# Optimization experiments

Hardware: AMD Instinct MI355X
Metric: run time of the kernel (lower is better)

Reference implementation:

```python
import jax, jax.numpy as jnp
import numpy as np

B, N, E, D = 8, 8192, 1024, 256

def setup_inputs() -> dict:
    key = jax.random.key(0)
    ks = jax.random.split(key, 6)
    obs = jax.random.normal(ks[0], (B, N, D), dtype=jnp.float32)
    mask_flat = (jax.random.uniform(ks[1], (B, N)) > 0.1).astype(jnp.float32)
    idx = jax.random.randint(ks[2], (B, N), 0, E)
    # incidence[b, e, n] = 1 iff obs n belongs to variable e (consistent with idx)
    incidence = jnp.transpose(jax.nn.one_hot(idx, E, dtype=jnp.float32), (0, 2, 1))
    # params (random instead of the degenerate zero-init so the math is exercised)
    w_m = jax.random.normal(ks[3], (1, 2 * D), dtype=jnp.float32) * 0.02
    b_m = jnp.full((1,), 3.0, dtype=jnp.float32)
    w_e = jax.random.normal(ks[4], (D // 4, 2 * D), dtype=jnp.float32) * 0.02
    b_e = jnp.zeros((D // 4,), dtype=jnp.float32)
    return {"obs": obs, "mask_flat": mask_flat,
            "variable_incidence_matrix": incidence,
            "variable_indices_flattened": idx,
            "w_m": w_m, "b_m": b_m, "w_e": w_e, "b_e": b_e}

def reference(obs, mask_flat, variable_incidence_matrix, variable_indices_flattened,
              w_m, b_m, w_e, b_e):
    # mean of member-obs embeddings per variable (hyperedge): (B,E,D)
    var_count = jnp.clip(variable_incidence_matrix.sum(-1, keepdims=True), 1.0, None)
    var_context = jnp.einsum('ben,bnd->bed', variable_incidence_matrix, obs) / var_count
    # gather each obs node's variable context: (B,N,D)
    obs_var_ctx = jax.vmap(lambda v, i: v[i])(var_context, variable_indices_flattened)
    membrane_input = jnp.concatenate([obs, obs - obs_var_ctx], axis=-1)  # (B,N,2D)
    membrane = (membrane_input @ w_m.T + b_m)[..., 0]                    # (B,N)
    g_n = jax.nn.sigmoid(membrane) * mask_flat
    e_n = (membrane_input @ w_e.T + b_e) * g_n[..., None] * mask_flat[..., None]
    return (g_n, e_n)
```

## Files before the change

### kernel.cpp

```cpp
#include <hip/hip_runtime.h>

#define B_ 8
#define N_ 8192
#define E_ 1024
#define ROWS (B_ * N_)
#define BE (B_ * E_)
#define NT 10
#define KT 8

typedef float  f32x4  __attribute__((ext_vector_type(4)));
typedef __bf16 bf16x8 __attribute__((ext_vector_type(8)));

#define SE16_OFF  0
#define SM16_OFF  (SE16_OFF + ROWS * 64 * 2)
#define Y2E_OFF   (SM16_OFF + ROWS * 2)
#define Y2M_OFF   (Y2E_OFF + ROWS * 64 * 2)
#define SEG_OFF   (Y2M_OFF + ROWS * 2)
#define ORD_OFF   (SEG_OFF + BE * 8)
#define WEF_OFF   (ORD_OFF + ROWS * 4)

__device__ inline float bflo(unsigned u) { return __uint_as_float(u << 16); }
__device__ inline float bfhi(unsigned u) { return __uint_as_float(u & 0xffff0000u); }

__global__ __launch_bounds__(1024) void bucketize_kernel(
    const int* __restrict__ idx, const float* __restrict__ we,
    const float* __restrict__ wm, char* __restrict__ ws) {

    const int bid = blockIdx.x;
    if (bid >= 8) {
        const int t = (bid - 8) * 1024 + threadIdx.x;
        if (t >= KT * NT * 64) return;
        __bf16* wef = (__bf16*)(ws + WEF_OFF);
        const int lane = t & 63;
        const int nt = (t >> 6) % NT;
        const int kt = t / (NT * 64);
        const int grp = nt / 5;
        const int r   = (nt % 5) * 16 + (lane & 15);
        const int k0  = kt * 32 + (lane >> 4) * 8;
        bf16x8 v;
#pragma unroll
        for (int i = 0; i < 8; ++i) {
            const int k = k0 + i;
            float f = 0.f;
            if (r < 64)       f = grp ? we[r * 512 + 256 + k] : we[r * 512 + k] + we[r * 512 + 256 + k];
            else if (r == 64) f = grp ? wm[256 + k]           : wm[k] + wm[256 + k];
            v[i] = (__bf16)f;
        }
        *(bf16x8*)(wef + (size_t)t * 8) = v;
        return;
    }

    __shared__ unsigned h[1024];
    __shared__ unsigned wpart[16];
    const int b = bid;
    const int t = threadIdx.x;
    const int lane = t & 63;
    const int w = t >> 6;

    h[t] = 0u;
    __syncthreads();

    unsigned my[8];
#pragma unroll
    for (int i = 0; i < 8; ++i) my[i] = (unsigned)idx[(b << 13) + (i << 10) + t];
#pragma unroll
    for (int i = 0; i < 8; ++i) atomicAdd(&h[my[i]], 1u);
    __syncthreads();

    const unsigned v = h[t];
    unsigned inc = v;
#pragma unroll
    for (int off = 1; off < 64; off <<= 1) {
        const unsigned u = __shfl_up(inc, off);
        if (lane >= off) inc += u;
    }
    if (lane == 63) wpart[w] = inc;
    __syncthreads();
    unsigned add = 0;
    for (int ww = 0; ww < w; ++ww) add += wpart[ww];
    const unsigned base = add + inc - v;

    ((uint2*)(ws + SEG_OFF))[(b << 10) + t] = (uint2){(unsigned)(b << 13) + base, v};
    __syncthreads();
    h[t] = base;
    __syncthreads();

    unsigned* order = (unsigned*)(ws + ORD_OFF);
#pragma unroll
    for (int i = 0; i < 8; ++i) {
        const unsigned p = atomicAdd(&h[my[i]], 1u);
        order[(b << 13) + p] = (unsigned)((b << 13) + (i << 10) + t);
    }
}

__global__ __launch_bounds__(256) void gemm_kernel(
    const float* __restrict__ obs, char* __restrict__ ws) {

    const __bf16*   wefg = (const __bf16*)(ws + WEF_OFF);
    const unsigned* ordu = (const unsigned*)(ws + ORD_OFF);
    const int tid = threadIdx.x;
    const int l   = tid & 63;
    const int pw0 = blockIdx.x * 128 + (tid >> 6) * 32;
    const int q8  = (l >> 4) << 3;

    const unsigned r0 = ordu[pw0 + (l & 15)];
    const unsigned r1 = ordu[pw0 + 16 + (l & 15)];

    f32x4 acc[2][NT];
#pragma unroll
    for (int a = 0; a < 2; ++a)
#pragma unroll
        for (int b = 0; b < NT; ++b) acc[a][b] = (f32x4){0.f, 0.f, 0.f, 0.f};

    const float* o0 = obs + (((size_t)r0) << 8) + q8;
    const float* o1 = obs + (((size_t)r1) << 8) + q8;

#pragma unroll
    for (int g = 0; g < KT; ++g) {
        const f32x4 oa0 = *(const f32x4*)(o0 + g * 32);
        const f32x4 ob0 = *(const f32x4*)(o0 + g * 32 + 4);
        const f32x4 oa1 = *(const f32x4*)(o1 + g * 32);
        const f32x4 ob1 = *(const f32x4*)(o1 + g * 32 + 4);
        bf16x8 A0, A1;
#pragma unroll
        for (int i = 0; i < 4; ++i) {
            A0[i] = (__bf16)oa0[i];  A0[4 + i] = (__bf16)ob0[i];
            A1[i] = (__bf16)oa1[i];  A1[4 + i] = (__bf16)ob1[i];
        }
#pragma unroll
        for (int nt = 0; nt < NT; ++nt) {
            const bf16x8 bb = *(const bf16x8*)(wefg + (size_t)(((g * NT + nt) << 6) + l) * 8);
            acc[0][nt] = __builtin_amdgcn_mfma_f32_16x16x32_bf16(A0, bb, acc[0][nt], 0, 0, 0);
            acc[1][nt] = __builtin_amdgcn_mfma_f32_16x16x32_bf16(A1, bb, acc[1][nt], 0, 0, 0);
        }
    }

    __bf16* sE  = (__bf16*)(ws + SE16_OFF);
    __bf16* sM  = (__bf16*)(ws + SM16_OFF);
    __bf16* y2e = (__bf16*)(ws + Y2E_OFF);
    __bf16* y2m = (__bf16*)(ws + Y2M_OFF);

    const int cgrp = (l >> 4) << 2;
    const int c16  = l & 15;
#pragma unroll
    for (int rt = 0; rt < 2; ++rt) {
#pragma unroll
        for (int j = 0; j < 4; ++j) {
            const int dp = pw0 + rt * 16 + cgrp + j;
#pragma unroll
            for (int nt = 0; nt < 4; ++nt) {
                sE [((size_t)dp << 6) + (nt << 4) + c16] = (__bf16)acc[rt][nt][j];
                y2e[((size_t)dp << 6) + (nt << 4) + c16] = (__bf16)acc[rt][5 + nt][j];
            }
            if (c16 == 0) {
                sM [dp] = (__bf16)acc[rt][4][j];
                y2m[dp] = (__bf16)acc[rt][9][j];
            }
        }
    }
}

__global__ __launch_bounds__(256) void tail_kernel(
    const float* __restrict__ mask, const float* __restrict__ bmp,
    const float* __restrict__ bep, const char* __restrict__ ws,
    float* __restrict__ out) {

    const int bucket = blockIdx.x * 4 + (threadIdx.x >> 6);
    const int l  = threadIdx.x & 63;
    const int lc = l & 31;
    const int hi = l >> 5;

    const uint2 sg = ((const uint2*)(ws + SEG_OFF))[bucket];
    const unsigned start = sg.x, len = sg.y;
    if (len == 0) return;

    const unsigned*       y2eu = (const unsigned*)(ws + Y2E_OFF);
    const unsigned short* y2m  = (const unsigned short*)(ws + Y2M_OFF);

    float ax = 0.f, ay = 0.f;
    for (unsigned i = hi; i < len; i += 2) {
        const unsigned u = y2eu[(size_t)(start + i) * 32 + lc];
        ax += bflo(u); ay += bfhi(u);
    }
    ax += __shfl_xor(ax, 32);
    ay += __shfl_xor(ay, 32);

    float mm = 0.f;
    for (unsigned i = l; i < len; i += 64) mm += bflo(y2m[start + i]);
#pragma unroll
    for (int off = 1; off < 64; off <<= 1) mm += __shfl_xor(mm, off);

    const float inv = 1.f / (float)len;
    const float meL = ax * inv, meH = ay * inv, mM = mm * inv;
    const float bm  = bmp[0];
    const float beL = bep[2 * lc], beH = bep[2 * lc + 1];

    const unsigned*       sEu  = (const unsigned*)(ws + SE16_OFF);
    const unsigned short* sM16 = (const unsigned short*)(ws + SM16_OFF);
    const unsigned*       ordu = (const unsigned*)(ws + ORD_OFF);

    for (unsigned i = hi; i < len; i += 2) {
        const unsigned d   = start + i;
        const unsigned row = ordu[d];
        const unsigned u   = sEu[(size_t)d * 32 + lc];
        const float sm = bflo(sM16[d]);
        const float mk = mask[row];
        const float m  = sm - mM + bm;
        const float g  = mk / (1.f + __expf(-m));
        float2 e;
        e.x = (bflo(u) - meL + beL) * g * mk;
        e.y = (bfhi(u) - meH + beH) * g * mk;
        *(float2*)(out + (size_t)ROWS + ((size_t)row << 6) + 2 * lc) = e;
        if (lc == 0) out[row] = g;
    }
}

extern "C" void kernel_launch(void* const* d_in, const int* in_sizes, int n_in,
                              void* d_out, int out_size, void* d_ws, size_t ws_size,
                              hipStream_t stream) {
    (void)in_sizes; (void)n_in; (void)out_size; (void)ws_size;
    const float* obs  = (const float*)d_in[0];
    const float* mask = (const float*)d_in[1];
    const int*   idx  = (const int*)d_in[3];
    const float* w_m  = (const float*)d_in[4];
    const float* b_m  = (const float*)d_in[5];
    const float* w_e  = (const float*)d_in[6];
    const float* b_e  = (const float*)d_in[7];

    char* ws = (char*)d_ws;

    bucketize_kernel<<<13, 1024, 0, stream>>>(idx, w_e, w_m, ws);
    gemm_kernel<<<ROWS / 128, 256, 0, stream>>>(obs, ws);
    tail_kernel<<<BE / 4, 256, 0, stream>>>(mask, b_m, b_e, ws, (float*)d_out);
}
```

Before: 45.95 us.

## Fuse segmented mean and epilogue into GEMM kernel with cross-block bucket reduction

Merges the tail kernel into the GEMM kernel. Per-bucket sums of the y2 projections are reduced in shared memory within each 128-row block, and the outputs are written directly for buckets fully contained in the block. Buckets that span block boundaries publish partial sums to a global slot array, and the last-arriving block (tracked with an atomic counter) finishes them serially. This removes the y2e/y2m workspace round-trip and one kernel launch. In exchange it adds a large LDS footprint, a serial loop for boundary buckets, and the correctness risk of relying on the last-block pattern.

```diff
diff --git a/kernel.cpp b/kernel.cpp
--- a/kernel.cpp
+++ b/kernel.cpp
@@ -13,18 +13,23 @@
 
 #define SE16_OFF  0
 #define SM16_OFF  (SE16_OFF + ROWS * 64 * 2)
-#define Y2E_OFF   (SM16_OFF + ROWS * 2)
-#define Y2M_OFF   (Y2E_OFF + ROWS * 64 * 2)
-#define SEG_OFF   (Y2M_OFF + ROWS * 2)
+#define SEG_OFF   (SM16_OFF + ROWS * 2)
 #define ORD_OFF   (SEG_OFF + BE * 8)
 #define WEF_OFF   (ORD_OFF + ROWS * 4)
-
-__device__ inline float bflo(unsigned u) { return __uint_as_float(u << 16); }
-__device__ inline float bfhi(unsigned u) { return __uint_as_float(u & 0xffff0000u); }
+#define GYS_OFF   (WEF_OFF + KT * NT * 64 * 8 * 2)
+#define GCNT_OFF  (GYS_OFF + (size_t)BE * 4 * 66 * 4)
+
+__device__ inline float bfu16(unsigned short u) { return __uint_as_float(((unsigned)u) << 16); }
 
 __global__ __launch_bounds__(1024) void bucketize_kernel(
     const int* __restrict__ idx, const float* __restrict__ we,
     const float* __restrict__ wm, char* __restrict__ ws) {
+
+    {
+        unsigned* gcnt = (unsigned*)(ws + GCNT_OFF);
+        const int gz = blockIdx.x * 1024 + threadIdx.x;
+        if (gz < BE) gcnt[gz] = 0u;
+    }
 
     const int bid = blockIdx.x;
     if (bid >= 8) {
@@ -93,18 +98,49 @@
     }
 }
 
-__global__ __launch_bounds__(256) void gemm_kernel(
-    const float* __restrict__ obs, char* __restrict__ ws) {
+__global__ __launch_bounds__(256) void gemm_fused_kernel(
+    const float* __restrict__ obs, const float* __restrict__ mask,
+    const int* __restrict__ idx, const float* __restrict__ bmp,
+    const float* __restrict__ bep, char* __restrict__ ws,
+    float* __restrict__ out) {
+
+    __shared__ float bsum[129][66];
 
     const __bf16*   wefg = (const __bf16*)(ws + WEF_OFF);
     const unsigned* ordu = (const unsigned*)(ws + ORD_OFF);
-    const int tid = threadIdx.x;
-    const int l   = tid & 63;
-    const int pw0 = blockIdx.x * 128 + (tid >> 6) * 32;
-    const int q8  = (l >> 4) << 3;
-
-    const unsigned r0 = ordu[pw0 + (l & 15)];
-    const unsigned r1 = ordu[pw0 + 16 + (l & 15)];
+    const uint2*    seg  = (const uint2*)(ws + SEG_OFF);
+    __bf16*   sE   = (__bf16*)(ws + SE16_OFF);
+    __bf16*   sM   = (__bf16*)(ws + SM16_OFF);
+    float*    gys  = (float*)(ws + GYS_OFF);
+    unsigned* gcnt = (unsigned*)(ws + GCNT_OFF);
+
+    const int tid    = threadIdx.x;
+    const int l      = tid & 63;
+    const int wv     = tid >> 6;
+    const int bstart = blockIdx.x * 128;
+    const int pw     = bstart + wv * 32;
+    const int c16    = l & 15;
+    const int cgrp   = (l >> 4) << 2;
+
+    for (int i = tid; i < 129 * 66; i += 256) (&bsum[0][0])[i] = 0.f;
+    __syncthreads();
+
+    unsigned row32 = 0; int bkt32 = -1; float mk32 = 0.f;
+    if (l < 32) {
+        row32 = ordu[pw + l];
+        bkt32 = (int)(((row32 >> 13) << 10) + (unsigned)idx[row32]);
+        mk32  = mask[row32];
+    }
+    const unsigned rA0 = __shfl(row32, c16);
+    const unsigned rA1 = __shfl(row32, 16 + c16);
+
+    const unsigned rowb0 = ordu[bstart];
+    const int kb0blk = (int)(((rowb0 >> 13) << 10) + (unsigned)idx[rowb0]);
+
+    const float bm = bmp[0];
+    float bel[4];
+#pragma unroll
+    for (int k = 0; k < 4; ++k) bel[k] = bep[(k << 4) + c16];
 
     f32x4 acc[2][NT];
 #pragma unroll
@@ -112,8 +148,9 @@
 #pragma unroll
         for (int b = 0; b < NT; ++b) acc[a][b] = (f32x4){0.f, 0.f, 0.f, 0.f};
 
-    const float* o0 = obs + (((size_t)r0) << 8) + q8;
-    const float* o1 = obs + (((size_t)r1) << 8) + q8;
+    const int q8 = (l >> 4) << 3;
+    const float* o0 = obs + (((size_t)rA0) << 8) + q8;
+    const float* o1 = obs + (((size_t)rA1) << 8) + q8;
 
 #pragma unroll
     for (int g = 0; g < KT; ++g) {
@@ -135,83 +172,124 @@
         }
     }
 
-    __bf16* sE  = (__bf16*)(ws + SE16_OFF);
-    __bf16* sM  = (__bf16*)(ws + SM16_OFF);
-    __bf16* y2e = (__bf16*)(ws + Y2E_OFF);
-    __bf16* y2m = (__bf16*)(ws + Y2M_OFF);
-
-    const int cgrp = (l >> 4) << 2;
-    const int c16  = l & 15;
-#pragma unroll
-    for (int rt = 0; rt < 2; ++rt) {
+    unsigned bmsk = 0;
+    float invrow[2][4] = {{0.f,0.f,0.f,0.f},{0.f,0.f,0.f,0.f}};
+    int s = 0;
+    while (s < 32) {
+        const int bkt = __shfl(bkt32, s);
+        const unsigned long long mrun = __ballot(bkt32 == bkt);
+        const unsigned long long mm = ~(mrun >> s);
+        const int e = s + (__ffsll((long long)mm) - 1);
+        const uint2 sg = seg[bkt];
+        const bool bnd = (sg.x < (unsigned)bstart) || (sg.x + sg.y > (unsigned)(bstart + 128));
+        const float invf = 1.f / (float)sg.y;
+        const int krel = bkt - kb0blk;
+
+        float s0 = 0.f, s1 = 0.f, s2 = 0.f, s3 = 0.f, sm5 = 0.f;
+#pragma unroll
+        for (int rt = 0; rt < 2; ++rt)
+#pragma unroll
+            for (int j = 0; j < 4; ++j) {
+                const int rr = rt * 16 + cgrp + j;
+                if (rr >= s && rr < e) {
+                    s0 += acc[rt][5][j]; s1 += acc[rt][6][j];
+                    s2 += acc[rt][7][j]; s3 += acc[rt][8][j];
+                    sm5 += acc[rt][9][j];
+                    invrow[rt][j] = invf;
+                    if (bnd) {
+                        bmsk |= 1u << (rt * 4 + j);
+                        const int pos = pw + rr;
+                        sE[((size_t)pos << 6) +  0 + c16] = (__bf16)acc[rt][0][j];
+                        sE[((size_t)pos << 6) + 16 + c16] = (__bf16)acc[rt][1][j];
+                        sE[((size_t)pos << 6) + 32 + c16] = (__bf16)acc[rt][2][j];
+                        sE[((size_t)pos << 6) + 48 + c16] = (__bf16)acc[rt][3][j];
+                        if (c16 == 0) sM[pos] = (__bf16)acc[rt][4][j];
+                    }
+                }
+            }
+        s0 += __shfl_xor(s0, 16); s0 += __shfl_xor(s0, 32);
+        s1 += __shfl_xor(s1, 16); s1 += __shfl_xor(s1, 32);
+        s2 += __shfl_xor(s2, 16); s2 += __shfl_xor(s2, 32);
+        s3 += __shfl_xor(s3, 16); s3 += __shfl_xor(s3, 32);
+        sm5 += __shfl_xor(sm5, 16); sm5 += __shfl_xor(sm5, 32);
+        if (l < 16) {
+            atomicAdd(&bsum[krel][ 0 + c16], s0);
+            atomicAdd(&bsum[krel][16 + c16], s1);
+            atomicAdd(&bsum[krel][32 + c16], s2);
+            atomicAdd(&bsum[krel][48 + c16], s3);
+            if (l == 0) atomicAdd(&bsum[krel][64], sm5);
+        }
+        s = e;
+    }
+    __syncthreads();
+
+#pragma unroll
+    for (int rt = 0; rt < 2; ++rt)
 #pragma unroll
         for (int j = 0; j < 4; ++j) {
-            const int dp = pw0 + rt * 16 + cgrp + j;
-#pragma unroll
-            for (int nt = 0; nt < 4; ++nt) {
-                sE [((size_t)dp << 6) + (nt << 4) + c16] = (__bf16)acc[rt][nt][j];
-                y2e[((size_t)dp << 6) + (nt << 4) + c16] = (__bf16)acc[rt][5 + nt][j];
+            const int rr = rt * 16 + cgrp + j;
+            const int krel = __shfl(bkt32, rr) - kb0blk;
+            const float invf = invrow[rt][j];
+            const float mM  = bsum[krel][64] * invf;
+            const float sMv = __shfl(acc[rt][4][j], l & 48);
+            const float mk  = __shfl(mk32, rr);
+            const unsigned row = __shfl(row32, rr);
+            const float g = mk / (1.f + __expf(-(sMv - mM + bm)));
+            if (!((bmsk >> (rt * 4 + j)) & 1u)) {
+                if (c16 == 0) out[row] = g;
+#pragma unroll
+                for (int k = 0; k < 4; ++k) {
+                    const float mean = bsum[krel][(k << 4) + c16] * invf;
+                    out[(size_t)ROWS + ((size_t)row << 6) + (k << 4) + c16] =
+                        (acc[rt][k][j] - mean + bel[k]) * g * mk;
+                }
             }
-            if (c16 == 0) {
-                sM [dp] = (__bf16)acc[rt][4][j];
-                y2m[dp] = (__bf16)acc[rt][9][j];
+        }
+
+    int kb = -1;
+    if (wv == 0) kb = kb0blk;
+    if (wv == 3) {
+        const int kbt = __shfl(bkt32, 31);
+        kb = (kbt == kb0blk) ? -1 : kbt;
+    }
+    if (kb >= 0) {
+        const uint2 sg = seg[kb];
+        if (sg.x < (unsigned)bstart || sg.x + sg.y > (unsigned)(bstart + 128)) {
+            const int krel   = kb - kb0blk;
+            const int firstb = (int)(sg.x >> 7);
+            const int nctr   = (int)((sg.x + sg.y - 1) >> 7) - firstb + 1;
+            const int slot   = (int)blockIdx.x - firstb;
+            float* slotp = gys + ((size_t)kb * 4 + slot) * 66;
+            slotp[l] = bsum[krel][l];
+            if (l == 0) slotp[64] = bsum[krel][64];
+            __threadfence();
+            unsigned old = 0;
+            if (l == 0) old = atomicAdd(&gcnt[kb], 1u);
+            old = __shfl(old, 0);
+            if ((int)old == nctr - 1) {
+                __threadfence();
+                float tot = 0.f, totM = 0.f;
+                for (int s2 = 0; s2 < nctr; ++s2) {
+                    const float* sp2 = gys + ((size_t)kb * 4 + s2) * 66;
+                    tot += sp2[l];
+                    if (l == 0) totM += sp2[64];
+                }
+                const float invf  = 1.f / (float)sg.y;
+                const float meanL = tot * invf;
+                const float meanM = __shfl(totM, 0) * invf;
+                const unsigned short* sEu = (const unsigned short*)sE;
+                const unsigned short* sMu = (const unsigned short*)sM;
+                for (unsigned p = sg.x; p < sg.x + sg.y; ++p) {
+                    const unsigned row = ordu[p];
+                    const float mk = mask[row];
+                    const float m  = bfu16(sMu[p]) - meanM + bm;
+                    const float g  = mk / (1.f + __expf(-m));
+                    out[(size_t)ROWS + ((size_t)row << 6) + l] =
+                        (bfu16(sEu[(size_t)p * 64 + l]) - meanL + bep[l]) * g * mk;
+                    if (l == 0) out[row] = g;
+                }
             }
         }
-    }
-}
-
-__global__ __launch_bounds__(256) void tail_kernel(
-    const float* __restrict__ mask, const float* __restrict__ bmp,
-    const float* __restrict__ bep, const char* __restrict__ ws,
-    float* __restrict__ out) {
-
-    const int bucket = blockIdx.x * 4 + (threadIdx.x >> 6);
-    const int l  = threadIdx.x & 63;
-    const int lc = l & 31;
-    const int hi = l >> 5;
-
-    const uint2 sg = ((const uint2*)(ws + SEG_OFF))[bucket];
-    const unsigned start = sg.x, len = sg.y;
-    if (len == 0) return;
-
-    const unsigned*       y2eu = (const unsigned*)(ws + Y2E_OFF);
-    const unsigned short* y2m  = (const unsigned short*)(ws + Y2M_OFF);
-
-    float ax = 0.f, ay = 0.f;
-    for (unsigned i = hi; i < len; i += 2) {
-        const unsigned u = y2eu[(size_t)(start + i) * 32 + lc];
-        ax += bflo(u); ay += bfhi(u);
-    }
-    ax += __shfl_xor(ax, 32);
-    ay += __shfl_xor(ay, 32);
-
-    float mm = 0.f;
-    for (unsigned i = l; i < len; i += 64) mm += bflo(y2m[start + i]);
-#pragma unroll
-    for (int off = 1; off < 64; off <<= 1) mm += __shfl_xor(mm, off);
-
-    const float inv = 1.f / (float)len;
-    const float meL = ax * inv, meH = ay * inv, mM = mm * inv;
-    const float bm  = bmp[0];
-    const float beL = bep[2 * lc], beH = bep[2 * lc + 1];
-
-    const unsigned*       sEu  = (const unsigned*)(ws + SE16_OFF);
-    const unsigned short* sM16 = (const unsigned short*)(ws + SM16_OFF);
-    const unsigned*       ordu = (const unsigned*)(ws + ORD_OFF);
-
-    for (unsigned i = hi; i < len; i += 2) {
-        const unsigned d   = start + i;
-        const unsigned row = ordu[d];
-        const unsigned u   = sEu[(size_t)d * 32 + lc];
-        const float sm = bflo(sM16[d]);
-        const float mk = mask[row];
-        const float m  = sm - mM + bm;
-        const float g  = mk / (1.f + __expf(-m));
-        float2 e;
-        e.x = (bflo(u) - meL + beL) * g * mk;
-        e.y = (bfhi(u) - meH + beH) * g * mk;
-        *(float2*)(out + (size_t)ROWS + ((size_t)row << 6) + 2 * lc) = e;
-        if (lc == 0) out[row] = g;
     }
 }
 
@@ -230,6 +308,6 @@
     char* ws = (char*)d_ws;
 
     bucketize_kernel<<<13, 1024, 0, stream>>>(idx, w_e, w_m, ws);
-    gemm_kernel<<<ROWS / 128, 256, 0, stream>>>(obs, ws);
-    tail_kernel<<<BE / 4, 256, 0, stream>>>(mask, b_m, b_e, ws, (float*)d_out);
+    gemm_fused_kernel<<<ROWS / 128, 256, 0, stream>>>(obs, mask, idx, b_m, b_e, ws,
+                                                      (float*)d_out);
 }
```

After: 113.5 us. 2.47x slower.
